# Performance work log

Measured on AMD Instinct MI355X. Metric: run time of the kernel, lower is better.

Reference implementation:

```python
import jax, jax.numpy as jnp
import numpy as np

D = 64          # d_manifold
R = 64          # n_rff
STRENGTH = 0.1
SIGMA = 0.5


def setup_inputs() -> dict:
    key = jax.random.key(0)
    ks = jax.random.split(key, 8)
    B, T = 8, 4096
    G = jax.random.normal(ks[0], (B, T, D, D), dtype=jnp.float32)
    coords = jax.random.normal(ks[1], (B, T, D), dtype=jnp.float32)
    # mass_net params: Linear(D, D) -> ReLU -> Linear(D, 1) -> Softplus
    w1 = jax.random.normal(ks[2], (D, D), dtype=jnp.float32) / np.sqrt(D)
    b1 = jnp.zeros((D,), dtype=jnp.float32)
    w2 = jax.random.normal(ks[3], (1, D), dtype=jnp.float32) / np.sqrt(D)
    b2 = jnp.zeros((1,), dtype=jnp.float32)
    # RFF buffers: W = randn(D, R)/sigma, b = rand(R)*2pi
    W = jax.random.normal(ks[4], (D, R), dtype=jnp.float32) / SIGMA
    b = jax.random.uniform(ks[5], (R,), dtype=jnp.float32) * 2.0 * np.pi
    return {"G": G, "coords": coords, "w1": w1, "b1": b1,
            "w2": w2, "b2": b2, "W": W, "b": b}


def reference(G, coords, w1, b1, w2, b2, W, b):
    # mass: [B, T, 1]
    h = jax.nn.relu(coords @ w1.T + b1)
    mass = jax.nn.softplus(h @ w2.T + b2)
    # RFF features phi(x) = sqrt(2/R) * cos(x @ W + b): [B, T, R]
    phi = jnp.sqrt(2.0 / R) * jnp.cos(coords @ W + b)
    # mass-weighted global sum over tokens: [B, 1, R]
    phi_sum = jnp.sum(phi * mass, axis=1, keepdims=True)
    # gravitational influence per token: [B, T, 1, 1]
    grav = jnp.sum(phi * phi_sum, axis=-1, keepdims=True)[..., None]
    I = jnp.eye(D, dtype=G.dtype)
    return G + STRENGTH * grav * I
```

## Files before the change

### kernel.cpp

```cpp
#include <hip/hip_runtime.h>
#include <math.h>

#define DM 64
#define RF 64
#define STRENGTH 0.1f
#define SQRT_2_OVER_R 0.17677669529663687f
#define NBATCH 8

__device__ __forceinline__ float wave_reduce_sum(float v) {
    #pragma unroll
    for (int off = 32; off > 0; off >>= 1)
        v += __shfl_xor(v, off, 64);
    return v;
}

__global__ __launch_bounds__(256) void gravity_pass1(
        const float* __restrict__ coords,
        const float* __restrict__ w1,
        const float* __restrict__ b1,
        const float* __restrict__ w2,
        const float* __restrict__ b2,
        const float* __restrict__ Wr,
        const float* __restrict__ br,
        float* __restrict__ phi_sum,
        int T) {
    const int lane = threadIdx.x & 63;
    const int wave = threadIdx.x >> 6;
    const int b    = blockIdx.y;
    const int wavesPerBatch = gridDim.x * 4;
    const int waveIdx = blockIdx.x * 4 + wave;

    float acc = 0.f;

    for (int t = waveIdx; t < T; t += wavesPerBatch) {
        const float* cptr = coords + ((size_t)b * T + t) * DM;
        float c = cptr[lane];
        float h  = b1[lane];
        float pd = br[lane];
        #pragma unroll
        for (int k = 0; k < DM; ++k) {
            float ck = __shfl(c, k, 64);
            h  = fmaf(ck, w1[lane * DM + k], h);
            pd = fmaf(ck, Wr[k * RF + lane], pd);
        }
        h = fmaxf(h, 0.f);
        float m = wave_reduce_sum(h * w2[lane]) + b2[0];
        m = fmaxf(m, 0.f) + log1pf(expf(-fabsf(m)));
        float phi = SQRT_2_OVER_R * cosf(pd);
        acc = fmaf(phi, m, acc);
    }

    __shared__ float s[4][RF];
    s[wave][lane] = acc;
    __syncthreads();
    if (wave == 0) {
        float v = s[0][lane] + s[1][lane] + s[2][lane] + s[3][lane];
        atomicAdd(&phi_sum[b * RF + lane], v);
    }
}

__global__ __launch_bounds__(256) void gravity_pass2(
        const float* __restrict__ coords,
        const float* __restrict__ Wr,
        const float* __restrict__ br,
        const float* __restrict__ phi_sum,
        float* __restrict__ grav,
        int total, int T) {
    const int lane  = threadIdx.x & 63;
    const int gwave = (int)((blockIdx.x * (size_t)blockDim.x + threadIdx.x) >> 6);
    if (gwave >= total) return;
    const int b = gwave / T;

    const float* cptr = coords + (size_t)gwave * DM;
    float c  = cptr[lane];
    float pd = br[lane];
    #pragma unroll
    for (int k = 0; k < DM; ++k) {
        float ck = __shfl(c, k, 64);
        pd = fmaf(ck, Wr[k * RF + lane], pd);
    }
    float phi = SQRT_2_OVER_R * cosf(pd);
    float v = wave_reduce_sum(phi * phi_sum[b * RF + lane]);
    if (lane == 0) grav[gwave] = STRENGTH * v;
}

__global__ __launch_bounds__(256) void gravity_pass3(
        const float4* __restrict__ G4,
        const float* __restrict__ grav,
        float4* __restrict__ out4,
        size_t n4) {
    size_t idx    = blockIdx.x * (size_t)blockDim.x + threadIdx.x;
    size_t stride = (size_t)gridDim.x * blockDim.x;
    for (; idx < n4; idx += stride) {
        float4 v = G4[idx];
        int token  = (int)(idx >> 10);
        int within = (int)(idx & 1023);
        int i  = within >> 4;
        int j0 = (within & 15) << 2;
        int d  = i - j0;
        if ((unsigned)d < 4u) {
            float g = grav[token];
            if      (d == 0) v.x += g;
            else if (d == 1) v.y += g;
            else if (d == 2) v.z += g;
            else             v.w += g;
        }
        out4[idx] = v;
    }
}

extern "C" void kernel_launch(void* const* d_in, const int* in_sizes, int n_in,
                              void* d_out, int out_size, void* d_ws, size_t ws_size,
                              hipStream_t stream) {
    const float* G      = (const float*)d_in[0];
    const float* coords = (const float*)d_in[1];
    const float* w1     = (const float*)d_in[2];
    const float* b1     = (const float*)d_in[3];
    const float* w2     = (const float*)d_in[4];
    const float* b2     = (const float*)d_in[5];
    const float* Wr     = (const float*)d_in[6];
    const float* br     = (const float*)d_in[7];
    float* out          = (float*)d_out;

    const int BT = in_sizes[1] / DM;
    const int B  = NBATCH;
    const int T  = BT / B;

    float* phi_sum = (float*)d_ws;
    float* grav    = (float*)d_ws + B * RF;

    hipMemsetAsync(d_ws, 0, (size_t)B * RF * sizeof(float), stream);

    dim3 g1(64, B);
    gravity_pass1<<<g1, 256, 0, stream>>>(coords, w1, b1, w2, b2, Wr, br,
                                          phi_sum, T);

    int blocks2 = (BT + 3) / 4;
    gravity_pass2<<<blocks2, 256, 0, stream>>>(coords, Wr, br, phi_sum, grav,
                                               BT, T);

    size_t n4 = (size_t)BT * DM * DM / 4;
    gravity_pass3<<<8192, 256, 0, stream>>>((const float4*)G, grav,
                                            (float4*)out, n4);
}
```

Baseline: 942.1 us.

## Cache phi from pass1 and fuse grav reduction into identity-add pass

Pass1 now keeps the w1 row and Wr column in registers and writes per-token phi to workspace. The separate grav kernel is removed: the final pass reads the stored phi, reduces it against phi_sum per token, and applies the diagonal add to G with nontemporal vector loads and stores, one block per four tokens. This saves a recompute of the RFF projection and a kernel launch, at the cost of a phi buffer write/read and higher register use in pass1. The main cost remains streaming G (about 537 MB read plus written).

```diff
diff --git a/kernel.cpp b/kernel.cpp
--- a/kernel.cpp
+++ b/kernel.cpp
@@ -6,6 +6,8 @@
 #define STRENGTH 0.1f
 #define SQRT_2_OVER_R 0.17677669529663687f
 #define NBATCH 8
+
+typedef float vf4 __attribute__((ext_vector_type(4)));
 
 __device__ __forceinline__ float wave_reduce_sum(float v) {
     #pragma unroll
@@ -22,6 +24,7 @@
         const float* __restrict__ b2,
         const float* __restrict__ Wr,
         const float* __restrict__ br,
+        float* __restrict__ phi_out,
         float* __restrict__ phi_sum,
         int T) {
     const int lane = threadIdx.x & 63;
@@ -30,23 +33,41 @@
     const int wavesPerBatch = gridDim.x * 4;
     const int waveIdx = blockIdx.x * 4 + wave;
 
+    float w1r[DM];
+    #pragma unroll
+    for (int q = 0; q < DM / 4; ++q) {
+        vf4 t = *reinterpret_cast<const vf4*>(w1 + (size_t)lane * DM + q * 4);
+        w1r[q * 4 + 0] = t[0];
+        w1r[q * 4 + 1] = t[1];
+        w1r[q * 4 + 2] = t[2];
+        w1r[q * 4 + 3] = t[3];
+    }
+    float wc[DM];
+    #pragma unroll
+    for (int k = 0; k < DM; ++k) wc[k] = Wr[k * RF + lane];
+    const float b1l = b1[lane];
+    const float brl = br[lane];
+    const float w2l = w2[lane];
+    const float b2s = b2[0];
+
     float acc = 0.f;
 
     for (int t = waveIdx; t < T; t += wavesPerBatch) {
-        const float* cptr = coords + ((size_t)b * T + t) * DM;
-        float c = cptr[lane];
-        float h  = b1[lane];
-        float pd = br[lane];
+        const size_t tok = (size_t)b * T + t;
+        float c = coords[tok * DM + lane];
+        float h  = b1l;
+        float pd = brl;
         #pragma unroll
         for (int k = 0; k < DM; ++k) {
             float ck = __shfl(c, k, 64);
-            h  = fmaf(ck, w1[lane * DM + k], h);
-            pd = fmaf(ck, Wr[k * RF + lane], pd);
+            h  = fmaf(ck, w1r[k], h);
+            pd = fmaf(ck, wc[k], pd);
         }
         h = fmaxf(h, 0.f);
-        float m = wave_reduce_sum(h * w2[lane]) + b2[0];
+        float m = wave_reduce_sum(h * w2l) + b2s;
         m = fmaxf(m, 0.f) + log1pf(expf(-fabsf(m)));
         float phi = SQRT_2_OVER_R * cosf(pd);
+        phi_out[tok * RF + lane] = phi;
         acc = fmaf(phi, m, acc);
     }
 
@@ -59,53 +80,44 @@
     }
 }
 
-__global__ __launch_bounds__(256) void gravity_pass2(
-        const float* __restrict__ coords,
-        const float* __restrict__ Wr,
-        const float* __restrict__ br,
+__global__ __launch_bounds__(256) void gravity_pass3(
+        const float* __restrict__ G,
+        const float* __restrict__ phi,
         const float* __restrict__ phi_sum,
-        float* __restrict__ grav,
-        int total, int T) {
-    const int lane  = threadIdx.x & 63;
-    const int gwave = (int)((blockIdx.x * (size_t)blockDim.x + threadIdx.x) >> 6);
-    if (gwave >= total) return;
-    const int b = gwave / T;
+        float* __restrict__ out,
+        int T) {
+    const int tid  = threadIdx.x;
+    const int lane = tid & 63;
+    const int w    = tid >> 6;
+    const int token = blockIdx.x * 4 + w;
+    const int b = token / T;
 
-    const float* cptr = coords + (size_t)gwave * DM;
-    float c  = cptr[lane];
-    float pd = br[lane];
+    __shared__ float gsh[4];
+    float v = phi[(size_t)token * RF + lane] * phi_sum[b * RF + lane];
+    v = wave_reduce_sum(v);
+    if (lane == 0) gsh[w] = STRENGTH * v;
+    __syncthreads();
+
+    const vf4* __restrict__ G4   = reinterpret_cast<const vf4*>(G);
+    vf4* __restrict__       out4 = reinterpret_cast<vf4*>(out);
+    const size_t base = (size_t)blockIdx.x * 4096;
+
     #pragma unroll
-    for (int k = 0; k < DM; ++k) {
-        float ck = __shfl(c, k, 64);
-        pd = fmaf(ck, Wr[k * RF + lane], pd);
-    }
-    float phi = SQRT_2_OVER_R * cosf(pd);
-    float v = wave_reduce_sum(phi * phi_sum[b * RF + lane]);
-    if (lane == 0) grav[gwave] = STRENGTH * v;
-}
-
-__global__ __launch_bounds__(256) void gravity_pass3(
-        const float4* __restrict__ G4,
-        const float* __restrict__ grav,
-        float4* __restrict__ out4,
-        size_t n4) {
-    size_t idx    = blockIdx.x * (size_t)blockDim.x + threadIdx.x;
-    size_t stride = (size_t)gridDim.x * blockDim.x;
-    for (; idx < n4; idx += stride) {
-        float4 v = G4[idx];
-        int token  = (int)(idx >> 10);
-        int within = (int)(idx & 1023);
-        int i  = within >> 4;
-        int j0 = (within & 15) << 2;
-        int d  = i - j0;
+    for (int j = 0; j < 16; ++j) {
+        const int il = j * 256 + tid;
+        vf4 vv = __builtin_nontemporal_load(&G4[base + il]);
+        const float g = gsh[j >> 2];
+        const int within = (j & 3) * 256 + tid;
+        const int i  = within >> 4;
+        const int j0 = (within & 15) << 2;
+        const int d  = i - j0;
         if ((unsigned)d < 4u) {
-            float g = grav[token];
-            if      (d == 0) v.x += g;
-            else if (d == 1) v.y += g;
-            else if (d == 2) v.z += g;
-            else             v.w += g;
+            if      (d == 0) vv[0] += g;
+            else if (d == 1) vv[1] += g;
+            else if (d == 2) vv[2] += g;
+            else             vv[3] += g;
         }
-        out4[idx] = v;
+        __builtin_nontemporal_store(vv, &out4[base + il]);
     }
 }
 
@@ -127,19 +139,13 @@
     const int T  = BT / B;
 
     float* phi_sum = (float*)d_ws;
-    float* grav    = (float*)d_ws + B * RF;
+    float* phi     = (float*)d_ws + B * RF;
 
     hipMemsetAsync(d_ws, 0, (size_t)B * RF * sizeof(float), stream);
 
     dim3 g1(64, B);
     gravity_pass1<<<g1, 256, 0, stream>>>(coords, w1, b1, w2, b2, Wr, br,
-                                          phi_sum, T);
+                                          phi, phi_sum, T);
 
-    int blocks2 = (BT + 3) / 4;
-    gravity_pass2<<<blocks2, 256, 0, stream>>>(coords, Wr, br, phi_sum, grav,
-                                               BT, T);
-
-    size_t n4 = (size_t)BT * DM * DM / 4;
-    gravity_pass3<<<8192, 256, 0, stream>>>((const float4*)G, grav,
-                                            (float4*)out, n4);
+    gravity_pass3<<<BT / 4, 256, 0, stream>>>(G, phi, phi_sum, out, T);
 }
```

Measured after the change: 909.0 us. 3.5% less time.
